# Optimization experiments

Measured on AMD Instinct MI355X. Metric: run time of the kernel, lower is better.

The kernel has to match this reference:

```python
import jax, jax.numpy as jnp
import numpy as np

T, B = 1024, 16384

def setup_inputs() -> dict:
    key = jax.random.key(0)
    ks = jax.random.split(key, 8)
    return {
        "inputs": jax.random.normal(ks[0], (T, B, 6), dtype=jnp.float32),
        "targets": jax.random.normal(ks[1], (T, B, 1), dtype=jnp.float32),
        "Wx": jax.random.normal(ks[2], (6, 6), dtype=jnp.float32) * 0.3,
        "Wu": jax.random.normal(ks[3], (6, 1), dtype=jnp.float32) * 0.3,
        "W1": jax.random.normal(ks[4], (20, 12), dtype=jnp.float32) * 0.3,
        "b1": jax.random.normal(ks[5], (20,), dtype=jnp.float32) * 0.1,
        "W2": jax.random.normal(ks[6], (1, 20), dtype=jnp.float32) * 0.3,
        "b2": jax.random.normal(ks[7], (1,), dtype=jnp.float32) * 0.1,
        "epoch": 10,
        "maxepoch": 100,
        "forceswitch": 2,
    }

def reference(inputs, targets, Wx, Wu, W1, b1, W2, b2, epoch, maxepoch, forceswitch):
    # forceswitch == 2 => deterministic teacher forcing: the feedback `output`
    # at step k is targets[k-1] for k > 0 and zeros at k = 0.
    assert forceswitch == 2
    Tlen, Bsz, _ = inputs.shape
    prev_out = jnp.concatenate(
        [jnp.zeros((1, Bsz, 1), dtype=inputs.dtype), targets[:-1]], axis=0
    )  # [T, B, 1]

    def step(db, xs):
        x_k, u_k = xs  # [B, 6], [B, 1]
        db = db @ Wx.T + u_k @ Wu.T                 # delay buffer update [B, 6]
        ni = jnp.concatenate([db, x_k], axis=-1)    # [B, 12]
        h = jnp.tanh(ni @ W1.T + b1)                # [B, 20]
        out = h @ W2.T + b2                         # [B, 1]
        return db, out

    db0 = jnp.zeros((Bsz, 6), dtype=inputs.dtype)
    _, outputs = jax.lax.scan(step, db0, (inputs, prev_out))
    return outputs  # [T, B, 1]
```

## Files before the change

kernel.cpp:

```cpp
#include <hip/hip_runtime.h>
#include <cstddef>

#define TT 1024
#define BB 16384
#define LC 32
#define CC (TT / LC)

__device__ __forceinline__ float fast_tanh(float x) {
    float e = __builtin_amdgcn_exp2f(x * 2.8853900817779268f);
    return fmaf(-2.0f, __builtin_amdgcn_rcpf(e + 1.0f), 1.0f);
}

__global__ __launch_bounds__(256) void k_phase1(
    const float* __restrict__ targets,
    const float* __restrict__ Wx,
    const float* __restrict__ Wu,
    float* __restrict__ v)
{
    const int b = blockIdx.x * 256 + threadIdx.x;
    const int c = blockIdx.y;
    float wx[6][6], wu[6];
#pragma unroll
    for (int i = 0; i < 6; ++i) {
        wu[i] = Wu[i];
#pragma unroll
        for (int j = 0; j < 6; ++j) wx[i][j] = Wx[i * 6 + j];
    }
    float db[6] = {0.f, 0.f, 0.f, 0.f, 0.f, 0.f};
    const int t0 = c * LC;
#pragma unroll 4
    for (int s = 0; s < LC; ++s) {
        const int t = t0 + s;
        float u = 0.0f;
        if (t > 0) u = targets[(size_t)(t - 1) * BB + b];
        float nd[6];
#pragma unroll
        for (int i = 0; i < 6; ++i) {
            float a = u * wu[i];
#pragma unroll
            for (int j = 0; j < 6; ++j) a = fmaf(db[j], wx[i][j], a);
            nd[i] = a;
        }
#pragma unroll
        for (int i = 0; i < 6; ++i) db[i] = nd[i];
    }
#pragma unroll
    for (int i = 0; i < 6; ++i) v[((size_t)c * 6 + i) * BB + b] = db[i];
}

__global__ __launch_bounds__(256) void k_phase2(
    const float* __restrict__ Wx,
    float* __restrict__ v)
{
    const int b = blockIdx.x * 256 + threadIdx.x;
    float M[6][6];
#pragma unroll
    for (int i = 0; i < 6; ++i)
#pragma unroll
        for (int j = 0; j < 6; ++j)
            M[j][i] = Wx[i * 6 + j];
    for (int it = 0; it < 5; ++it) {
        float P[6][6];
#pragma unroll
        for (int i = 0; i < 6; ++i)
#pragma unroll
            for (int j = 0; j < 6; ++j) {
                float a = 0.0f;
#pragma unroll
                for (int k = 0; k < 6; ++k) a = fmaf(M[i][k], M[k][j], a);
                P[i][j] = a;
            }
#pragma unroll
        for (int i = 0; i < 6; ++i)
#pragma unroll
            for (int j = 0; j < 6; ++j) M[i][j] = P[i][j];
    }
    float db[6] = {0.f, 0.f, 0.f, 0.f, 0.f, 0.f};
    for (int c = 0; c < CC; ++c) {
        float vv[6];
#pragma unroll
        for (int i = 0; i < 6; ++i) {
            const size_t idx = ((size_t)c * 6 + i) * BB + b;
            vv[i] = v[idx];
            v[idx] = db[i];
        }
        float nd[6];
#pragma unroll
        for (int i = 0; i < 6; ++i) {
            float a = vv[i];
#pragma unroll
            for (int j = 0; j < 6; ++j) a = fmaf(db[j], M[j][i], a);
            nd[i] = a;
        }
#pragma unroll
        for (int i = 0; i < 6; ++i) db[i] = nd[i];
    }
}

__global__ __launch_bounds__(256, 3) void k_phase3(
    const float* __restrict__ inputs,
    const float* __restrict__ targets,
    const float* __restrict__ Wxg,
    const float* __restrict__ Wug,
    const float* __restrict__ W1g,
    const float* __restrict__ b1g,
    const float* __restrict__ W2g,
    const float* __restrict__ b2g,
    const float* __restrict__ dbs,
    float* __restrict__ out)
{
    const int tid = threadIdx.x;
    const int q   = tid & 3;
    const int b   = blockIdx.x * 64 + (tid >> 2);
    const int c   = blockIdx.y;
    const int m0  = q * 5;

    float wx[6][6], wu[6];
#pragma unroll
    for (int i = 0; i < 6; ++i) {
        wu[i] = Wug[i];
#pragma unroll
        for (int j = 0; j < 6; ++j) wx[i][j] = Wxg[i * 6 + j];
    }
    const float vb2 = b2g[0];

    float w1l[5][12];
    float b1l[5], w2l[5];
#pragma unroll
    for (int p = 0; p < 5; ++p) {
#pragma unroll
        for (int j = 0; j < 12; ++j) w1l[p][j] = W1g[(m0 + p) * 12 + j];
        b1l[p] = b1g[m0 + p];
        w2l[p] = W2g[m0 + p];
    }

    float db[6];
#pragma unroll
    for (int i = 0; i < 6; ++i) db[i] = dbs[((size_t)c * 6 + i) * BB + b];

    const int t0 = c * LC;
    const float* xptr = inputs + ((size_t)t0 * BB + b) * 6;
    const float* tptr = targets + (size_t)t0 * BB + b;
    float* optr = out + (size_t)t0 * BB + b;

    float u_cur = (t0 == 0) ? 0.0f : tptr[-(ptrdiff_t)BB];
    float2 x0 = *(const float2*)(xptr);
    float2 x1 = *(const float2*)(xptr + 2);
    float2 x2 = *(const float2*)(xptr + 4);

    for (int s = 0; s < LC; ++s) {
        float u_nxt = 0.0f;
        float2 n0 = x0, n1 = x1, n2 = x2;
        if (s + 1 < LC) {
            u_nxt = *tptr;
            const float* xn = xptr + (size_t)BB * 6;
            n0 = *(const float2*)(xn);
            n1 = *(const float2*)(xn + 2);
            n2 = *(const float2*)(xn + 4);
        }

        float nd[6];
#pragma unroll
        for (int i = 0; i < 6; ++i) {
            float a = u_cur * wu[i];
#pragma unroll
            for (int j = 0; j < 6; ++j) a = fmaf(db[j], wx[i][j], a);
            nd[i] = a;
        }
#pragma unroll
        for (int i = 0; i < 6; ++i) db[i] = nd[i];

        const float ni[12] = {db[0], db[1], db[2], db[3], db[4], db[5],
                              x0.x, x0.y, x1.x, x1.y, x2.x, x2.y};

        float acc[5];
#pragma unroll
        for (int p = 0; p < 5; ++p) acc[p] = b1l[p];
#pragma unroll
        for (int j = 0; j < 12; ++j) {
            const float nij = ni[j];
#pragma unroll
            for (int p = 0; p < 5; ++p) acc[p] = fmaf(w1l[p][j], nij, acc[p]);
        }

        float o = 0.0f;
#pragma unroll
        for (int p = 0; p < 5; ++p) o = fmaf(w2l[p], fast_tanh(acc[p]), o);

        o += __shfl_xor(o, 1, 64);
        o += __shfl_xor(o, 2, 64);
        if (q == 0) *optr = o + vb2;

        u_cur = u_nxt; x0 = n0; x1 = n1; x2 = n2;
        xptr += (size_t)BB * 6;
        tptr += BB;
        optr += BB;
    }
}

extern "C" void kernel_launch(void* const* d_in, const int* in_sizes, int n_in,
                              void* d_out, int out_size, void* d_ws, size_t ws_size,
                              hipStream_t stream) {
    (void)in_sizes; (void)n_in; (void)out_size; (void)ws_size;
    const float* inputs  = (const float*)d_in[0];
    const float* targets = (const float*)d_in[1];
    const float* Wx = (const float*)d_in[2];
    const float* Wu = (const float*)d_in[3];
    const float* W1 = (const float*)d_in[4];
    const float* b1 = (const float*)d_in[5];
    const float* W2 = (const float*)d_in[6];
    const float* b2 = (const float*)d_in[7];
    float* out = (float*)d_out;
    float* v   = (float*)d_ws;

    dim3 blk(256);
    dim3 g1(BB / 256, CC);
    hipLaunchKernelGGL(k_phase1, g1, blk, 0, stream, targets, Wx, Wu, v);
    hipLaunchKernelGGL(k_phase2, dim3(BB / 256), blk, 0, stream, Wx, v);
    dim3 g3(BB / 64, CC);
    hipLaunchKernelGGL(k_phase3, g3, blk, 0, stream,
                       inputs, targets, Wx, Wu, W1, b1, W2, b2, v, out);
}
```

Baseline: 775.4 us.

## Split phase3 into fp16 delay-buffer expansion and a fully parallel MLP kernel

When the workspace is large enough, phase 3 is replaced by two kernels. The first replays each chunk's delay-buffer recurrence and stores every per-timestep state packed as fp16 pairs. The second evaluates the MLP independently for each (t, b), with one thread per batch element computing all 20 hidden units. This removes the 4-thread split with its shuffle reduction and the serial per-chunk loop in the MLP stage. In exchange it adds a large intermediate write and read (about 200MB) and reduces the precision of the delay-buffer inputs to fp16.

```diff
diff --git a/kernel.cpp b/kernel.cpp
--- a/kernel.cpp
+++ b/kernel.cpp
@@ -1,10 +1,13 @@
 #include <hip/hip_runtime.h>
 #include <cstddef>
+#include <cstdint>
 
 #define TT 1024
 #define BB 16384
 #define LC 32
 #define CC (TT / LC)
+
+typedef __fp16 h2 __attribute__((ext_vector_type(2)));
 
 __device__ __forceinline__ float fast_tanh(float x) {
     float e = __builtin_amdgcn_exp2f(x * 2.8853900817779268f);
@@ -95,6 +98,93 @@
 #pragma unroll
         for (int i = 0; i < 6; ++i) db[i] = nd[i];
     }
+}
+
+__global__ __launch_bounds__(256) void k_expand(
+    const float* __restrict__ targets,
+    const float* __restrict__ Wxg,
+    const float* __restrict__ Wug,
+    const float* __restrict__ dbs,
+    uint32_t* __restrict__ dbh)
+{
+    const int b = blockIdx.x * 256 + threadIdx.x;
+    const int c = blockIdx.y;
+    float wx[6][6], wu[6];
+#pragma unroll
+    for (int i = 0; i < 6; ++i) {
+        wu[i] = Wug[i];
+#pragma unroll
+        for (int j = 0; j < 6; ++j) wx[i][j] = Wxg[i * 6 + j];
+    }
+    float db[6];
+#pragma unroll
+    for (int i = 0; i < 6; ++i) db[i] = dbs[((size_t)c * 6 + i) * BB + b];
+
+    const int t0 = c * LC;
+#pragma unroll 4
+    for (int s = 0; s < LC; ++s) {
+        const int t = t0 + s;
+        float u = 0.0f;
+        if (t > 0) u = targets[(size_t)(t - 1) * BB + b];
+        float nd[6];
+#pragma unroll
+        for (int i = 0; i < 6; ++i) {
+            float a = u * wu[i];
+#pragma unroll
+            for (int j = 0; j < 6; ++j) a = fmaf(db[j], wx[i][j], a);
+            nd[i] = a;
+        }
+#pragma unroll
+        for (int i = 0; i < 6; ++i) db[i] = nd[i];
+#pragma unroll
+        for (int k = 0; k < 3; ++k) {
+            h2 p = __builtin_amdgcn_cvt_pkrtz(db[2 * k], db[2 * k + 1]);
+            dbh[((size_t)t * 3 + k) * BB + b] = __builtin_bit_cast(uint32_t, p);
+        }
+    }
+}
+
+__global__ __launch_bounds__(256) void k_mlp(
+    const float* __restrict__ inputs,
+    const uint32_t* __restrict__ dbh,
+    const float* __restrict__ W1g,
+    const float* __restrict__ b1g,
+    const float* __restrict__ W2g,
+    const float* __restrict__ b2g,
+    float* __restrict__ out)
+{
+    const int b = blockIdx.x * 256 + threadIdx.x;
+    const int t = blockIdx.y;
+
+    float ni[12];
+#pragma unroll
+    for (int k = 0; k < 3; ++k) {
+        uint32_t u = dbh[((size_t)t * 3 + k) * BB + b];
+        h2 p = __builtin_bit_cast(h2, u);
+        ni[2 * k]     = (float)p.x;
+        ni[2 * k + 1] = (float)p.y;
+    }
+    const float* xp = inputs + ((size_t)t * BB + b) * 6;
+    float2 x0 = *(const float2*)(xp);
+    float2 x1 = *(const float2*)(xp + 2);
+    float2 x2 = *(const float2*)(xp + 4);
+    ni[6] = x0.x; ni[7] = x0.y; ni[8] = x1.x;
+    ni[9] = x1.y; ni[10] = x2.x; ni[11] = x2.y;
+
+    float acc[20];
+#pragma unroll
+    for (int m = 0; m < 20; ++m) acc[m] = b1g[m];
+#pragma unroll
+    for (int j = 0; j < 12; ++j) {
+        const float nij = ni[j];
+#pragma unroll
+        for (int m = 0; m < 20; ++m) acc[m] = fmaf(W1g[m * 12 + j], nij, acc[m]);
+    }
+    float o = b2g[0];
+#pragma unroll
+    for (int m = 0; m < 20; ++m) o = fmaf(W2g[m], fast_tanh(acc[m]), o);
+
+    out[(size_t)t * BB + b] = o;
 }
 
 __global__ __launch_bounds__(256, 3) void k_phase3(
@@ -158,7 +248,6 @@
             n1 = *(const float2*)(xn + 2);
             n2 = *(const float2*)(xn + 4);
         }
-
         float nd[6];
 #pragma unroll
         for (int i = 0; i < 6; ++i) {
@@ -172,7 +261,6 @@
 
         const float ni[12] = {db[0], db[1], db[2], db[3], db[4], db[5],
                               x0.x, x0.y, x1.x, x1.y, x2.x, x2.y};
-
         float acc[5];
 #pragma unroll
         for (int p = 0; p < 5; ++p) acc[p] = b1l[p];
@@ -182,11 +270,9 @@
 #pragma unroll
             for (int p = 0; p < 5; ++p) acc[p] = fmaf(w1l[p][j], nij, acc[p]);
         }
-
         float o = 0.0f;
 #pragma unroll
         for (int p = 0; p < 5; ++p) o = fmaf(w2l[p], fast_tanh(acc[p]), o);
-
         o += __shfl_xor(o, 1, 64);
         o += __shfl_xor(o, 2, 64);
         if (q == 0) *optr = o + vb2;
@@ -201,7 +287,7 @@
 extern "C" void kernel_launch(void* const* d_in, const int* in_sizes, int n_in,
                               void* d_out, int out_size, void* d_ws, size_t ws_size,
                               hipStream_t stream) {
-    (void)in_sizes; (void)n_in; (void)out_size; (void)ws_size;
+    (void)in_sizes; (void)n_in; (void)out_size;
     const float* inputs  = (const float*)d_in[0];
     const float* targets = (const float*)d_in[1];
     const float* Wx = (const float*)d_in[2];
@@ -211,13 +297,26 @@
     const float* W2 = (const float*)d_in[6];
     const float* b2 = (const float*)d_in[7];
     float* out = (float*)d_out;
-    float* v   = (float*)d_ws;
+
+    float* v = (float*)d_ws;
+    const size_t v_elems   = (size_t)CC * 6 * BB;
+    const size_t dbh_elems = (size_t)TT * 3 * BB;
+    const size_t need      = (v_elems + dbh_elems) * 4;
 
     dim3 blk(256);
     dim3 g1(BB / 256, CC);
     hipLaunchKernelGGL(k_phase1, g1, blk, 0, stream, targets, Wx, Wu, v);
     hipLaunchKernelGGL(k_phase2, dim3(BB / 256), blk, 0, stream, Wx, v);
-    dim3 g3(BB / 64, CC);
-    hipLaunchKernelGGL(k_phase3, g3, blk, 0, stream,
-                       inputs, targets, Wx, Wu, W1, b1, W2, b2, v, out);
-}
+
+    if (ws_size >= need) {
+        uint32_t* dbh = (uint32_t*)(v + v_elems);
+        hipLaunchKernelGGL(k_expand, g1, blk, 0, stream, targets, Wx, Wu, v, dbh);
+        dim3 g3(BB / 256, TT);
+        hipLaunchKernelGGL(k_mlp, g3, blk, 0, stream,
+                           inputs, dbh, W1, b1, W2, b2, out);
+    } else {
+        dim3 g3(BB / 64, CC);
+        hipLaunchKernelGGL(k_phase3, g3, blk, 0, stream,
+                           inputs, targets, Wx, Wu, W1, b1, W2, b2, v, out);
+    }
+}
```

Measured after the change: 729.2 us. -6.0%, faster.

## Assign one thread per batch element in phase 3 with LDS-broadcast MLP weights

Applied to the files above, without the earlier changes.

Replaces the four-lanes-per-element split of the output MLP with one thread computing all 20 hidden units, reading W1/b1/W2 from shared memory. This removes the redundant recurrence update computed by every lane, the cross-lane shuffle reduction, and the strided output stores. In exchange each thread does four times the tanh and FMA work serially and adds many LDS reads, and the occupancy hint is dropped.

```diff
diff --git a/kernel.cpp b/kernel.cpp
--- a/kernel.cpp
+++ b/kernel.cpp
@@ -1,5 +1,6 @@
 #include <hip/hip_runtime.h>
 #include <cstddef>
+#include <cstdint>
 
 #define TT 1024
 #define BB 16384
@@ -97,7 +98,7 @@
     }
 }
 
-__global__ __launch_bounds__(256, 3) void k_phase3(
+__global__ __launch_bounds__(256) void k_fused(
     const float* __restrict__ inputs,
     const float* __restrict__ targets,
     const float* __restrict__ Wxg,
@@ -109,11 +110,16 @@
     const float* __restrict__ dbs,
     float* __restrict__ out)
 {
+    __shared__ float w1s[20][12];
+    __shared__ float b1s[20];
+    __shared__ float w2s[20];
+
     const int tid = threadIdx.x;
-    const int q   = tid & 3;
-    const int b   = blockIdx.x * 64 + (tid >> 2);
-    const int c   = blockIdx.y;
-    const int m0  = q * 5;
+    if (tid < 240) w1s[tid / 12][tid % 12] = W1g[tid];
+    if (tid < 20) {
+        b1s[tid] = b1g[tid];
+        w2s[tid] = W2g[tid];
+    }
 
     float wx[6][6], wu[6];
 #pragma unroll
@@ -124,19 +130,14 @@
     }
     const float vb2 = b2g[0];
 
-    float w1l[5][12];
-    float b1l[5], w2l[5];
-#pragma unroll
-    for (int p = 0; p < 5; ++p) {
-#pragma unroll
-        for (int j = 0; j < 12; ++j) w1l[p][j] = W1g[(m0 + p) * 12 + j];
-        b1l[p] = b1g[m0 + p];
-        w2l[p] = W2g[m0 + p];
-    }
+    const int b = blockIdx.x * 256 + tid;
+    const int c = blockIdx.y;
 
     float db[6];
 #pragma unroll
     for (int i = 0; i < 6; ++i) db[i] = dbs[((size_t)c * 6 + i) * BB + b];
+
+    __syncthreads();
 
     const int t0 = c * LC;
     const float* xptr = inputs + ((size_t)t0 * BB + b) * 6;
@@ -148,6 +149,7 @@
     float2 x1 = *(const float2*)(xptr + 2);
     float2 x2 = *(const float2*)(xptr + 4);
 
+#pragma unroll 1
     for (int s = 0; s < LC; ++s) {
         float u_nxt = 0.0f;
         float2 n0 = x0, n1 = x1, n2 = x2;
@@ -159,6 +161,8 @@
             n2 = *(const float2*)(xn + 4);
         }
 
+        asm volatile("" ::: "memory");
+
         float nd[6];
 #pragma unroll
         for (int i = 0; i < 6; ++i) {
@@ -173,23 +177,22 @@
         const float ni[12] = {db[0], db[1], db[2], db[3], db[4], db[5],
                               x0.x, x0.y, x1.x, x1.y, x2.x, x2.y};
 
-        float acc[5];
-#pragma unroll
-        for (int p = 0; p < 5; ++p) acc[p] = b1l[p];
-#pragma unroll
-        for (int j = 0; j < 12; ++j) {
-            const float nij = ni[j];
-#pragma unroll
-            for (int p = 0; p < 5; ++p) acc[p] = fmaf(w1l[p][j], nij, acc[p]);
-        }
-
         float o = 0.0f;
 #pragma unroll
-        for (int p = 0; p < 5; ++p) o = fmaf(w2l[p], fast_tanh(acc[p]), o);
-
-        o += __shfl_xor(o, 1, 64);
-        o += __shfl_xor(o, 2, 64);
-        if (q == 0) *optr = o + vb2;
+        for (int m = 0; m < 20; ++m) {
+            const float4 wa = *(const float4*)(&w1s[m][0]);
+            const float4 wb = *(const float4*)(&w1s[m][4]);
+            const float4 wc = *(const float4*)(&w1s[m][8]);
+            float a = b1s[m];
+            a = fmaf(wa.x, ni[0], a);  a = fmaf(wa.y, ni[1], a);
+            a = fmaf(wa.z, ni[2], a);  a = fmaf(wa.w, ni[3], a);
+            a = fmaf(wb.x, ni[4], a);  a = fmaf(wb.y, ni[5], a);
+            a = fmaf(wb.z, ni[6], a);  a = fmaf(wb.w, ni[7], a);
+            a = fmaf(wc.x, ni[8], a);  a = fmaf(wc.y, ni[9], a);
+            a = fmaf(wc.z, ni[10], a); a = fmaf(wc.w, ni[11], a);
+            o = fmaf(w2s[m], fast_tanh(a), o);
+        }
+        *optr = o + vb2;
 
         u_cur = u_nxt; x0 = n0; x1 = n1; x2 = n2;
         xptr += (size_t)BB * 6;
@@ -217,7 +220,6 @@
     dim3 g1(BB / 256, CC);
     hipLaunchKernelGGL(k_phase1, g1, blk, 0, stream, targets, Wx, Wu, v);
     hipLaunchKernelGGL(k_phase2, dim3(BB / 256), blk, 0, stream, Wx, v);
-    dim3 g3(BB / 64, CC);
-    hipLaunchKernelGGL(k_phase3, g3, blk, 0, stream,
+    hipLaunchKernelGGL(k_fused, g1, blk, 0, stream,
                        inputs, targets, Wx, Wu, W1, b1, W2, b2, v, out);
 }
```

Result: faster. 671.8 us (-13.4%).
